# Optimization experiments

Measured on AMD Instinct MI355X. Metric: run time of the kernel, lower is better.

Reference implementation:

```python
import jax, jax.numpy as jnp
import numpy as np

DEPTH = 8
IN_FEATURES = 512
OUT_FEATURES = 64
BATCH = 4096
LEAF_COUNT = 2 ** DEPTH          # 256
GATE_COUNT = LEAF_COUNT - 1      # 255


def tree_paths(depth):
    """Replicates the torch loop: for each leaf i, the gate index visited at each
    level j and whether the path takes the right branch (bit '1' -> 1-gating)."""
    leaves = 2 ** depth
    idx = np.zeros((depth, leaves), dtype=np.int32)
    bit = np.zeros((depth, leaves), dtype=bool)
    for i in range(leaves):
        bits = np.binary_repr(i, width=depth)
        index = 1
        for j in range(depth):
            idx[j, i] = index - 1
            bit[j, i] = (bits[j] == '1')
            index = 2 * index + (1 if bits[j] == '1' else 0)
    return idx, bit


def setup_inputs() -> dict:
    key = jax.random.key(0)
    kx, kg, kp = jax.random.split(key, 3)
    x = jax.random.normal(kx, (BATCH, IN_FEATURES), dtype=jnp.float32)
    # kaiming_normal_(nonlinearity='sigmoid') on [gate_count, in_features]: gain=1,
    # fan_in = in_features -> std = 1/sqrt(in_features); stored transposed.
    gw = jax.random.normal(kg, (IN_FEATURES, GATE_COUNT), dtype=jnp.float32) / np.sqrt(IN_FEATURES)
    gb = jnp.zeros((GATE_COUNT,), dtype=jnp.float32)
    # kaiming_normal_(nonlinearity='linear') on [out*leaf, in]: std = 1/sqrt(in_features),
    # reshaped to [out, leaf, in] then permuted to [out, in, leaf].
    pw = jax.random.normal(kp, (OUT_FEATURES, IN_FEATURES, LEAF_COUNT), dtype=jnp.float32) / np.sqrt(IN_FEATURES)
    pb = jnp.zeros((OUT_FEATURES, LEAF_COUNT), dtype=jnp.float32)
    idx, bit = tree_paths(DEPTH)
    return {
        'x': x, 'gw': gw, 'gb': gb, 'pw': pw, 'pb': pb,
        'leaf_idx': jnp.asarray(idx), 'leaf_bit': jnp.asarray(bit),
    }


def reference(x, gw, gb, pw, pb, leaf_idx, leaf_bit):
    # gatings: [B, gate_count]
    gatings = jax.nn.sigmoid(x @ gw + gb)
    # gather gate prob along each leaf path: [B, depth, leaf_count]
    g_sel = gatings[:, leaf_idx]
    branch = jnp.where(leaf_bit[None], 1.0 - g_sel, g_sel)
    leaf_probs = jnp.prod(branch, axis=1)            # [B, leaf_count]
    # per-leaf projection of x, plus bias: [B, out, leaf_count]
    per_leaf = jnp.einsum('bi,oil->bol', x, pw) + pb[None]
    # mixture over leaves: [B, out]
    return jnp.einsum('bol,bl->bo', per_leaf, leaf_probs)
```

## Files before the change

kernel.cpp:

```cpp
#include <hip/hip_runtime.h>
#include <cstdint>
#include <cstddef>

#define GATES 255

typedef __attribute__((ext_vector_type(8))) short bf16x8;
typedef __attribute__((ext_vector_type(4))) float f32x4;

__device__ __forceinline__ short f2bf(float f) {
  union { float f; uint32_t u; } c; c.f = f;
  uint32_t r = c.u + 0x7FFFu + ((c.u >> 16) & 1u);
  return (short)(r >> 16);
}

#define GLOAD16(gp, lp) __builtin_amdgcn_global_load_lds( \
    (const __attribute__((address_space(1))) uint32_t*)(gp), \
    (__attribute__((address_space(3))) uint32_t*)(lp), 16, 0, 0)

__global__ __launch_bounds__(256) void k_prep(const float* __restrict__ x,
                                              short* __restrict__ xb,
                                              const float* __restrict__ gw,
                                              short* __restrict__ gwt,
                                              const float* __restrict__ pw,
                                              short* __restrict__ pwt) {
  __shared__ short t[64][65];
  const int bx = blockIdx.x;
  const int tid = threadIdx.x;

  if (bx < 2048) {
    const int i = bx * 256 + tid;
    const float4 v = ((const float4*)x)[i];
    short4 s;
    s.x = f2bf(v.x); s.y = f2bf(v.y); s.z = f2bf(v.z); s.w = f2bf(v.w);
    ((short4*)xb)[i] = s;
    return;
  }

  const int c = tid & 63, r0 = tid >> 6;

  if (bx < 2080) {
    const int b2 = bx - 2048;
    const int ib = b2 >> 2, gb = b2 & 3;
    const int i0 = ib << 6, g0 = gb << 6;
#pragma unroll
    for (int rr = 0; rr < 16; ++rr) {
      const int i = rr * 4 + r0;
      const int g = g0 + c;
      t[i][c] = (g < GATES) ? f2bf(gw[(size_t)(i0 + i) * GATES + g]) : (short)0;
    }
    __syncthreads();
#pragma unroll
    for (int rr = 0; rr < 16; ++rr) {
      const int gg = rr * 4 + r0;
      gwt[(size_t)(g0 + gg) * 512 + i0 + c] = t[c][gg];
    }
    return;
  }

  const int b2 = bx - 2080;
  const int o = b2 >> 5;
  const int ib = (b2 >> 2) & 7;
  const int lb = b2 & 3;
  const int i0 = ib << 6, l0 = lb << 6;
  const float* src = pw + ((size_t)o * 512 + i0) * 256 + l0;
#pragma unroll
  for (int rr = 0; rr < 16; ++rr) {
    const int i = rr * 4 + r0;
    t[i][c] = f2bf(src[(size_t)i * 256 + c]);
  }
  __syncthreads();
  short* dst = pwt + ((size_t)o * 256 + l0) * 512 + i0;
#pragma unroll
  for (int rr = 0; rr < 16; ++rr) {
    const int ll = rr * 4 + r0;
    dst[(size_t)ll * 512 + c] = t[c][ll];
  }
}

__global__ __launch_bounds__(256, 1) void k_gate(const short* __restrict__ xb,
                                                 const short* __restrict__ gwt,
                                                 const float* __restrict__ gb,
                                                 float* __restrict__ p) {
  __shared__ short a_lds[64 * 64];
  __shared__ short b_lds[256 * 64];
  __shared__ float gs[64][260];

  const int b0 = blockIdx.x << 6;
  const int tid = threadIdx.x;
  const int lane = tid & 63;
  const int w = tid >> 6;
  const int wr = w >> 1, wc = w & 1;

  const short* Ab = xb + (size_t)b0 * 512;

  f32x4 acc[2][8];
#pragma unroll
  for (int mf = 0; mf < 2; ++mf)
#pragma unroll
    for (int nf = 0; nf < 8; ++nf) {
      acc[mf][nf][0] = 0.f; acc[mf][nf][1] = 0.f;
      acc[mf][nf][2] = 0.f; acc[mf][nf][3] = 0.f;
    }

  for (int s = 0; s < 8; ++s) {
    const int i0 = s << 6;
    __syncthreads();
#pragma unroll
    for (int sw = 0; sw < 2; ++sw) {
      const int chunk = sw * 256 + tid;
      const int r = chunk >> 3, c = (chunk & 7) << 3;
      GLOAD16(Ab + (size_t)r * 512 + i0 + c, a_lds + chunk * 8);
    }
#pragma unroll
    for (int sw = 0; sw < 8; ++sw) {
      const int chunk = sw * 256 + tid;
      const int r = chunk >> 3, c = (chunk & 7) << 3;
      GLOAD16(gwt + (size_t)r * 512 + i0 + c, b_lds + chunk * 8);
    }
    __syncthreads();
#pragma unroll
    for (int kk = 0; kk < 2; ++kk) {
      const int kb = (kk << 5) + ((lane >> 4) << 3);
      bf16x8 af[2], bfr[8];
#pragma unroll
      for (int mf = 0; mf < 2; ++mf) {
        const int row = (wr << 5) + (mf << 4) + (lane & 15);
        af[mf] = *(const bf16x8*)(a_lds + row * 64 + kb);
      }
#pragma unroll
      for (int nf = 0; nf < 8; ++nf) {
        const int row = (wc << 7) + (nf << 4) + (lane & 15);
        bfr[nf] = *(const bf16x8*)(b_lds + row * 64 + kb);
      }
#pragma unroll
      for (int mf = 0; mf < 2; ++mf)
#pragma unroll
        for (int nf = 0; nf < 8; ++nf)
          acc[mf][nf] = __builtin_amdgcn_mfma_f32_16x16x32_bf16(
              af[mf], bfr[nf], acc[mf][nf], 0, 0, 0);
    }
  }

  const int grp = lane >> 4, lcol = lane & 15;
#pragma unroll
  for (int nf = 0; nf < 8; ++nf) {
    const int g = (wc << 7) + (nf << 4) + lcol;
    const float bias = (g < GATES) ? gb[g] : 0.f;
#pragma unroll
    for (int mf = 0; mf < 2; ++mf)
#pragma unroll
      for (int rg = 0; rg < 4; ++rg) {
        const int bl = (wr << 5) + (mf << 4) + (grp << 2) + rg;
        const float z = acc[mf][nf][rg] + bias;
        gs[bl][g] = 1.f / (1.f + __expf(-z));
      }
  }
  __syncthreads();

  const int l = tid;
  for (int r = 0; r < 64; ++r) {
    float prob = 1.f;
    int index = 1;
#pragma unroll
    for (int j = 0; j < 8; ++j) {
      const int bit = (l >> (7 - j)) & 1;
      const float gg = gs[r][index - 1];
      prob *= bit ? (1.f - gg) : gg;
      index = 2 * index + bit;
    }
    p[(size_t)(b0 + r) * 256 + l] = prob;
  }
}

__global__ __launch_bounds__(256, 2) void k_main(const short* __restrict__ xb,
                                                 const short* __restrict__ pwt,
                                                 const float* __restrict__ p,
                                                 const float* __restrict__ pb,
                                                 float* __restrict__ out) {
  __shared__ short a_lds[128 * 64];
  __shared__ short b_lds[256 * 64];

  const int bx = blockIdx.x;
  const int o = bx >> 5;
  const int bm0 = (bx & 31) << 7;
  const int tid = threadIdx.x;
  const int lane = tid & 63;
  const int w = tid >> 6;
  const int wr = w >> 1;
  const int wc = w & 1;

  const short* Ab = xb + (size_t)bm0 * 512;
  const short* Bb = pwt + (size_t)o * (256 * 512);

  f32x4 acc[4][8];
#pragma unroll
  for (int mf = 0; mf < 4; ++mf)
#pragma unroll
    for (int nf = 0; nf < 8; ++nf) {
      acc[mf][nf][0] = 0.f; acc[mf][nf][1] = 0.f;
      acc[mf][nf][2] = 0.f; acc[mf][nf][3] = 0.f;
    }

  for (int s = 0; s < 8; ++s) {
    const int i0 = s << 6;
    __syncthreads();
#pragma unroll
    for (int sw = 0; sw < 4; ++sw) {
      const int c = sw * 256 + tid;
      const int r = c >> 3;
      const int gblk = (c & 7) ^ (r & 7);
      GLOAD16(Ab + (size_t)r * 512 + i0 + (gblk << 3), a_lds + c * 8);
    }
#pragma unroll
    for (int sw = 0; sw < 8; ++sw) {
      const int c = sw * 256 + tid;
      const int r = c >> 3;
      const int gblk = (c & 7) ^ (r & 7);
      GLOAD16(Bb + (size_t)r * 512 + i0 + (gblk << 3), b_lds + c * 8);
    }
    __syncthreads();
#pragma unroll
    for (int kk = 0; kk < 2; ++kk) {
      const int kblk = (kk << 2) + (lane >> 4);
      bf16x8 af[4], bfr[8];
#pragma unroll
      for (int mf = 0; mf < 4; ++mf) {
        const int row = (wr << 6) + (mf << 4) + (lane & 15);
        af[mf] = *(const bf16x8*)(a_lds + row * 64 + ((kblk ^ (row & 7)) << 3));
      }
#pragma unroll
      for (int nf = 0; nf < 8; ++nf) {
        const int row = (wc << 7) + (nf << 4) + (lane & 15);
        bfr[nf] = *(const bf16x8*)(b_lds + row * 64 + ((kblk ^ (row & 7)) << 3));
      }
#pragma unroll
      for (int mf = 0; mf < 4; ++mf)
#pragma unroll
        for (int nf = 0; nf < 8; ++nf)
          acc[mf][nf] = __builtin_amdgcn_mfma_f32_16x16x32_bf16(
              af[mf], bfr[nf], acc[mf][nf], 0, 0, 0);
    }
  }

  __syncthreads();
  float* red = (float*)a_lds;
  const int grp = lane >> 4;
  const int lcol = lane & 15;
  float pbv[8];
#pragma unroll
  for (int nf = 0; nf < 8; ++nf)
    pbv[nf] = pb[(size_t)o * 256 + (wc << 7) + (nf << 4) + lcol];
#pragma unroll
  for (int mf = 0; mf < 4; ++mf) {
#pragma unroll
    for (int rg = 0; rg < 4; ++rg) {
      const int bl = (wr << 6) + (mf << 4) + (grp << 2) + rg;
      const int b = bm0 + bl;
      float v = 0.f;
#pragma unroll
      for (int nf = 0; nf < 8; ++nf) {
        const int l = (wc << 7) + (nf << 4) + lcol;
        v += (acc[mf][nf][rg] + pbv[nf]) * p[(size_t)b * 256 + l];
      }
      v += __shfl_xor(v, 1);
      v += __shfl_xor(v, 2);
      v += __shfl_xor(v, 4);
      v += __shfl_xor(v, 8);
      if (lcol == 0) red[wc * 128 + bl] = v;
    }
  }
  __syncthreads();
  if (tid < 128) {
    out[(size_t)(bm0 + tid) * 64 + o] = red[tid] + red[128 + tid];
  }
}

extern "C" void kernel_launch(void* const* d_in, const int* in_sizes, int n_in,
                              void* d_out, int out_size, void* d_ws, size_t ws_size,
                              hipStream_t stream) {
  (void)in_sizes; (void)n_in; (void)out_size; (void)ws_size;
  const float* x  = (const float*)d_in[0];
  const float* gw = (const float*)d_in[1];
  const float* gb = (const float*)d_in[2];
  const float* pw = (const float*)d_in[3];
  const float* pb = (const float*)d_in[4];
  float* out = (float*)d_out;

  char* ws = (char*)d_ws;
  short* xbuf = (short*)(ws);
  short* gwt  = (short*)(ws + ((size_t)4 << 20));
  short* pwt  = (short*)(ws + ((size_t)4 << 20) + (256 << 10));
  float* p    = (float*)(ws + ((size_t)20 << 20) + (256 << 10));

  k_prep<<<4128, 256, 0, stream>>>(x, xbuf, gw, gwt, pw, pwt);
  k_gate<<<64, 256, 0, stream>>>(xbuf, gwt, gb, p);
  k_main<<<2048, 256, 0, stream>>>(xbuf, pwt, p, pb, out);
}
```

Before: 119.3 us.

## Double-buffer LDS tiles with a 32-wide K step to overlap loads and MFMA

The main GEMM loop now uses two LDS buffers holding 32-wide K slices instead of one 64-wide buffer. Each iteration issues the async global-to-LDS loads for the next slice before running the MFMAs on the current one, with a single barrier per step. The aim is to hide global load latency behind compute. In exchange there are twice as many steps. The narrower 4-chunk XOR swizzle on 64-byte rows may cause more LDS bank conflicts.

New measurement: 144.6 us. +21.2%, slower.

```diff
diff --git a/kernel.cpp b/kernel.cpp
--- a/kernel.cpp
+++ b/kernel.cpp
@@ -177,8 +177,8 @@
                                                  const float* __restrict__ p,
                                                  const float* __restrict__ pb,
                                                  float* __restrict__ out) {
-  __shared__ short a_lds[128 * 64];
-  __shared__ short b_lds[256 * 64];
+  __shared__ short a_lds[2][128 * 32];
+  __shared__ short b_lds[2][256 * 32];
 
   const int bx = blockIdx.x;
   const int o = bx >> 5;
@@ -201,49 +201,54 @@
       acc[mf][nf][2] = 0.f; acc[mf][nf][3] = 0.f;
     }
 
-  for (int s = 0; s < 8; ++s) {
-    const int i0 = s << 6;
+  auto stage = [&](int buf, int t) {
+    const int i0 = t << 5;
+#pragma unroll
+    for (int j = 0; j < 2; ++j) {
+      const int c = j * 256 + tid;
+      const int r = c >> 2;
+      const int gblk = (c & 3) ^ (r & 3);
+      GLOAD16(Ab + (size_t)r * 512 + i0 + (gblk << 3), &a_lds[buf][c * 8]);
+    }
+#pragma unroll
+    for (int j = 0; j < 4; ++j) {
+      const int c = j * 256 + tid;
+      const int r = c >> 2;
+      const int gblk = (c & 3) ^ (r & 3);
+      GLOAD16(Bb + (size_t)r * 512 + i0 + (gblk << 3), &b_lds[buf][c * 8]);
+    }
+  };
+
+  auto compute = [&](int buf) {
+    const int kq = lane >> 4;
+    bf16x8 af[4], bfr[8];
+#pragma unroll
+    for (int mf = 0; mf < 4; ++mf) {
+      const int row = (wr << 6) + (mf << 4) + (lane & 15);
+      af[mf] = *(const bf16x8*)(&a_lds[buf][row * 32 + ((kq ^ (row & 3)) << 3)]);
+    }
+#pragma unroll
+    for (int nf = 0; nf < 8; ++nf) {
+      const int row = (wc << 7) + (nf << 4) + (lane & 15);
+      bfr[nf] = *(const bf16x8*)(&b_lds[buf][row * 32 + ((kq ^ (row & 3)) << 3)]);
+    }
+#pragma unroll
+    for (int mf = 0; mf < 4; ++mf)
+#pragma unroll
+      for (int nf = 0; nf < 8; ++nf)
+        acc[mf][nf] = __builtin_amdgcn_mfma_f32_16x16x32_bf16(
+            af[mf], bfr[nf], acc[mf][nf], 0, 0, 0);
+  };
+
+  stage(0, 0);
+  __syncthreads();
+  for (int t = 0; t < 16; ++t) {
+    if (t < 15) stage((t + 1) & 1, t + 1);
+    compute(t & 1);
     __syncthreads();
-#pragma unroll
-    for (int sw = 0; sw < 4; ++sw) {
-      const int c = sw * 256 + tid;
-      const int r = c >> 3;
-      const int gblk = (c & 7) ^ (r & 7);
-      GLOAD16(Ab + (size_t)r * 512 + i0 + (gblk << 3), a_lds + c * 8);
-    }
-#pragma unroll
-    for (int sw = 0; sw < 8; ++sw) {
-      const int c = sw * 256 + tid;
-      const int r = c >> 3;
-      const int gblk = (c & 7) ^ (r & 7);
-      GLOAD16(Bb + (size_t)r * 512 + i0 + (gblk << 3), b_lds + c * 8);
-    }
-    __syncthreads();
-#pragma unroll
-    for (int kk = 0; kk < 2; ++kk) {
-      const int kblk = (kk << 2) + (lane >> 4);
-      bf16x8 af[4], bfr[8];
-#pragma unroll
-      for (int mf = 0; mf < 4; ++mf) {
-        const int row = (wr << 6) + (mf << 4) + (lane & 15);
-        af[mf] = *(const bf16x8*)(a_lds + row * 64 + ((kblk ^ (row & 7)) << 3));
-      }
-#pragma unroll
-      for (int nf = 0; nf < 8; ++nf) {
-        const int row = (wc << 7) + (nf << 4) + (lane & 15);
-        bfr[nf] = *(const bf16x8*)(b_lds + row * 64 + ((kblk ^ (row & 7)) << 3));
-      }
-#pragma unroll
-      for (int mf = 0; mf < 4; ++mf)
-#pragma unroll
-        for (int nf = 0; nf < 8; ++nf)
-          acc[mf][nf] = __builtin_amdgcn_mfma_f32_16x16x32_bf16(
-              af[mf], bfr[nf], acc[mf][nf], 0, 0, 0);
-    }
-  }
-
-  __syncthreads();
-  float* red = (float*)a_lds;
+  }
+
+  float* red = (float*)&a_lds[0][0];
   const int grp = lane >> 4;
   const int lcol = lane & 15;
   float pbv[8];
```
